# Optimization experiments

Measured on AMD Instinct MI355X. Metric: run time of the kernel, lower is better.

The kernel has to match this reference:

```python
import jax, jax.numpy as jnp
import numpy as np

B, S, D = 8, 4096, 64
NEG = 10000.0


def setup_inputs() -> dict:
    key = jax.random.key(0)
    k1, k2, k3, k4 = jax.random.split(key, 4)
    query = jax.random.normal(k1, (B, S, D), dtype=jnp.float32)
    k_ = jax.random.normal(k2, (B, S, D), dtype=jnp.float32)
    v_ = jax.random.normal(k3, (B, S, D), dtype=jnp.float32)
    # padding mask [B, Sk]: mostly valid, tail padded for some rows
    lens = jax.random.randint(k4, (B,), S // 2, S + 1)
    mask = jnp.arange(S)[None, :] < lens[:, None]
    return {"query": query, "key": k_, "value": v_, "mask": mask}


def reference(query, key, value, mask):
    d = query.shape[-1]
    scale = 1.0 / jnp.sqrt(jnp.asarray(d, dtype=query.dtype))
    # e: [B, Sq, Sk]
    e = jnp.einsum("bqd,bkd->bqk", query, key) * scale
    # causal (history_only) mask: key index > query index gets -10000
    q_idx = jnp.arange(query.shape[1])[:, None]
    k_idx = jnp.arange(key.shape[1])[None, :]
    e = e - NEG * (k_idx > q_idx).astype(e.dtype)[None, :, :]
    # padding mask [B, 1, Sk]
    e = e - NEG * (1.0 - mask.astype(e.dtype))[:, None, :]
    attention = jax.nn.softmax(e, axis=-1)
    return jnp.einsum("bqk,bkd->bqd", attention, value)
```

## Files before the change

kernel.cpp:

```cpp
#include <hip/hip_runtime.h>
#include <hip/hip_bf16.h>

#define B_N 8
#define S_N 4096
#define D_N 64
#define NQT 64
#define TILE_BYTES 8192
#define SLOT_BYTES 4352

typedef __attribute__((ext_vector_type(8))) short bf16x8;
typedef __attribute__((ext_vector_type(4))) float f32x4;
typedef __attribute__((ext_vector_type(16))) float f32x16;
typedef unsigned uint2v __attribute__((ext_vector_type(2)));
typedef unsigned uint4v __attribute__((ext_vector_type(4)));

__device__ __forceinline__ float fast_exp2(float x) {
#if __has_builtin(__builtin_amdgcn_exp2f)
  return __builtin_amdgcn_exp2f(x);
#else
  return exp2f(x);
#endif
}

__device__ __forceinline__ unsigned f2bf_u(float x) {
  __hip_bfloat16 h = __float2bfloat16(x);
  return (unsigned)__builtin_bit_cast(unsigned short, h);
}
__device__ __forceinline__ unsigned pack2(float a, float b) {
  return f2bf_u(a) | (f2bf_u(b) << 16);
}

__device__ __forceinline__ void pl32swap(unsigned& a, unsigned& b) {
#if __has_builtin(__builtin_amdgcn_permlane32_swap)
  uint2v r = __builtin_amdgcn_permlane32_swap(a, b, false, false);
  a = r[0];
  b = r[1];
#else
  asm volatile("v_permlane32_swap_b32 %0, %1" : "+v"(a), "+v"(b));
#endif
}
__device__ __forceinline__ float xhalf_sum(float x) {
  unsigned a = __builtin_bit_cast(unsigned, x), b = a;
  pl32swap(a, b);
  return __builtin_bit_cast(float, a) + __builtin_bit_cast(float, b);
}

__global__ void __launch_bounds__(256)
lens_kernel(const unsigned* __restrict__ mask, int* __restrict__ lens) {
  int b = blockIdx.x, tid = threadIdx.x;
  unsigned first = mask[0];
  int cnt = 0;
  if (first == 0x01010101u) {
    const unsigned char* m = ((const unsigned char*)mask) + (size_t)b * S_N;
    for (int i = tid; i < S_N; i += 256) cnt += (m[i] != 0);
  } else if (first == 0x3F800000u) {
    const float* m = ((const float*)mask) + (size_t)b * S_N;
    for (int i = tid; i < S_N; i += 256) cnt += (m[i] != 0.0f);
  } else {
    const int* m = ((const int*)mask) + (size_t)b * S_N;
    for (int i = tid; i < S_N; i += 256) cnt += (m[i] != 0);
  }
#pragma unroll
  for (int off = 32; off > 0; off >>= 1) cnt += __shfl_down(cnt, off);
  __shared__ int acc[4];
  if ((tid & 63) == 0) acc[tid >> 6] = cnt;
  __syncthreads();
  if (tid == 0) lens[b] = acc[0] + acc[1] + acc[2] + acc[3];
}

__global__ void __launch_bounds__(256)
prep_kernel(const float* __restrict__ K, const float* __restrict__ V,
            char* __restrict__ Ks, char* __restrict__ VTs) {
  __shared__ float vl[64][72];
  const int bt = blockIdx.x, tid = threadIdx.x;
  const float* Kt = K + (size_t)bt * 4096;
  const float* Vt = V + (size_t)bt * 4096;
  char* Ko = Ks + (size_t)bt * TILE_BYTES;
  char* Vo = VTs + (size_t)bt * TILE_BYTES;
#pragma unroll
  for (int i = 0; i < 2; ++i) {
    int c = tid + i * 256;
    int r = c >> 3, j = c & 7;
    f32x4 a = *(const f32x4*)(Kt + r * 64 + j * 8);
    f32x4 b4 = *(const f32x4*)(Kt + r * 64 + j * 8 + 4);
    union { bf16x8 v; unsigned u[4]; } pk;
    pk.u[0] = pack2(a[0], a[1]);   pk.u[1] = pack2(a[2], a[3]);
    pk.u[2] = pack2(b4[0], b4[1]); pk.u[3] = pack2(b4[2], b4[3]);
    *(bf16x8*)(Ko + ((r >> 5) * 4 + (j >> 1)) * 1024 + (j & 1) * 512 +
               (r & 31) * 16) = pk.v;
    f32x4 va = *(const f32x4*)(Vt + r * 64 + j * 8);
    f32x4 vb = *(const f32x4*)(Vt + r * 64 + j * 8 + 4);
#pragma unroll
    for (int e = 0; e < 4; ++e) vl[j * 8 + e][r] = va[e];
#pragma unroll
    for (int e = 0; e < 4; ++e) vl[j * 8 + 4 + e][r] = vb[e];
  }
  __syncthreads();
#pragma unroll
  for (int i = 0; i < 2; ++i) {
    int c = tid + i * 256;
    int d = c >> 3, j = c & 7;
    f32x4 fa = *(const f32x4*)(&vl[d][j * 8]);
    f32x4 fb = *(const f32x4*)(&vl[d][j * 8 + 4]);
    union { bf16x8 v; unsigned u[4]; } pk;
    pk.u[0] = pack2(fa[0], fa[1]); pk.u[1] = pack2(fa[2], fa[3]);
    pk.u[2] = pack2(fb[0], fb[1]); pk.u[3] = pack2(fb[2], fb[3]);
    *(bf16x8*)(Vo + ((d >> 5) * 4 + (j >> 1)) * 1024 + (j & 1) * 512 +
               (d & 31) * 16) = pk.v;
  }
}

__global__ void __launch_bounds__(256, 2)
attn_kernel(const float* __restrict__ Qg, const char* __restrict__ Ks,
            const char* __restrict__ VTs, const int* __restrict__ lens,
            float* __restrict__ Og, char* __restrict__ parts,
            int M, int U) {
  const int tid = threadIdx.x;
  const int lane = tid & 63;
  const int w = tid >> 6;
  const int bid = blockIdx.x;
  const int b = bid & 7;
  const int u2 = (bid >> 3) * 4 + w;
  const int ws = u2 & 1;
  const int u = (U - 1) - (u2 >> 1);
  int a = 0;
  while ((M * (a + 1) * (a + 2)) / 2 <= u) ++a;
  const int v = u - (M * a * (a + 1)) / 2;
  const int qt = a * M + v / (a + 1);
  const int s = v - (v / (a + 1)) * (a + 1);
  const int kq = a + 1;

  const int q0 = qt * 64;
  const int len = lens[b];
  int nt = (len + 63) >> 6;
  if (qt + 1 < nt) nt = qt + 1;
  const int beg = s * M;
  int cnt = nt - beg;
  if (cnt > M) cnt = M;
  if (cnt < 0) cnt = 0;

  const int q31 = lane & 31;
  const int h = lane >> 5;
  const int qg = q0 + ws * 32 + q31;

  const char* Kb = Ks + (size_t)(b * NQT) * TILE_BYTES;
  const char* Vb = VTs + (size_t)(b * NQT) * TILE_BYTES;

  constexpr float CS = 0.125f * 1.4426950408889634f;
  bf16x8 qf[4];
#pragma unroll
  for (int c = 0; c < 4; ++c) {
    const float* src = Qg + ((size_t)(b * S_N) + qg) * D_N + c * 16 + h * 8;
    f32x4 aa = *(const f32x4*)src;
    f32x4 b4 = *(const f32x4*)(src + 4);
    union { bf16x8 v; unsigned u[4]; } pk;
    pk.u[0] = pack2(aa[0] * CS, aa[1] * CS);
    pk.u[1] = pack2(aa[2] * CS, aa[3] * CS);
    pk.u[2] = pack2(b4[0] * CS, b4[1] * CS);
    pk.u[3] = pack2(b4[2] * CS, b4[3] * CS);
    qf[c] = pk.v;
  }

  f32x16 ot0 = {}, ot1 = {};
  float l = 0.0f;

  bf16x8 ka[8];
  if (cnt > 0) {
    const char* Kt = Kb + (size_t)beg * TILE_BYTES + lane * 16;
#pragma unroll
    for (int c = 0; c < 8; ++c) ka[c] = *(const bf16x8*)(Kt + c * 1024);
  }

  for (int j = 0; j < cnt; ++j) {
    const int t = beg + j;

    f32x16 s0, s1;
#pragma unroll
    for (int i = 0; i < 16; ++i) { s0[i] = -8.0f; s1[i] = -8.0f; }
#pragma unroll
    for (int c = 0; c < 4; ++c) {
      s0 = __builtin_amdgcn_mfma_f32_32x32x16_bf16(ka[c], qf[c], s0, 0, 0, 0);
      s1 = __builtin_amdgcn_mfma_f32_32x32x16_bf16(ka[4 + c], qf[c], s1, 0, 0, 0);
    }

    bf16x8 vv[8];
    const char* Vt2 = Vb + (size_t)t * TILE_BYTES + lane * 16;
#pragma unroll
    for (int c = 0; c < 8; ++c) vv[c] = *(const bf16x8*)(Vt2 + c * 1024);

    if (j + 1 < cnt) {
      const char* Kn = Kb + (size_t)(t + 1) * TILE_BYTES + lane * 16;
#pragma unroll
      for (int c = 0; c < 8; ++c) ka[c] = *(const bf16x8*)(Kn + c * 1024);
    }

    const int kv0 = t * 64;
    if (t == qt || kv0 + 64 > len) {
#pragma unroll
      for (int g = 0; g < 4; ++g)
#pragma unroll
        for (int jj = 0; jj < 4; ++jj) {
          int kl = 8 * g + 4 * h + jj;
          if (kv0 + kl > qg || kv0 + kl >= len) s0[g * 4 + jj] = -10000.0f;
          if (kv0 + 32 + kl > qg || kv0 + 32 + kl >= len) s1[g * 4 + jj] = -10000.0f;
        }
    }

    float ps0 = 0.f, ps1 = 0.f, ps2 = 0.f, ps3 = 0.f;
#pragma unroll
    for (int g = 0; g < 4; ++g) {
      s0[4 * g + 0] = fast_exp2(s0[4 * g + 0]); ps0 += s0[4 * g + 0];
      s0[4 * g + 1] = fast_exp2(s0[4 * g + 1]); ps1 += s0[4 * g + 1];
      s0[4 * g + 2] = fast_exp2(s0[4 * g + 2]); ps2 += s0[4 * g + 2];
      s0[4 * g + 3] = fast_exp2(s0[4 * g + 3]); ps3 += s0[4 * g + 3];
      s1[4 * g + 0] = fast_exp2(s1[4 * g + 0]); ps0 += s1[4 * g + 0];
      s1[4 * g + 1] = fast_exp2(s1[4 * g + 1]); ps1 += s1[4 * g + 1];
      s1[4 * g + 2] = fast_exp2(s1[4 * g + 2]); ps2 += s1[4 * g + 2];
      s1[4 * g + 3] = fast_exp2(s1[4 * g + 3]); ps3 += s1[4 * g + 3];
    }
    l += xhalf_sum((ps0 + ps1) + (ps2 + ps3));

    unsigned opk0[4][2], opk1[4][2];
#pragma unroll
    for (int g = 0; g < 4; ++g) {
      opk0[g][0] = pack2(s0[4 * g + 0], s0[4 * g + 1]);
      opk0[g][1] = pack2(s0[4 * g + 2], s0[4 * g + 3]);
      opk1[g][0] = pack2(s1[4 * g + 0], s1[4 * g + 1]);
      opk1[g][1] = pack2(s1[4 * g + 2], s1[4 * g + 3]);
    }
    bf16x8 pb[4];
#pragma unroll
    for (int c = 0; c < 4; ++c) {
      const unsigned(*o)[2] = (c < 2) ? opk0 : opk1;
      const int g0 = 2 * (c & 1), g1 = g0 + 1;
      unsigned a0 = o[g0][0], b0 = o[g1][0];
      unsigned a1 = o[g0][1], b1 = o[g1][1];
      pl32swap(a0, b0);
      pl32swap(a1, b1);
      union { bf16x8 v; unsigned u[4]; } pk;
      pk.u[0] = a0; pk.u[1] = a1; pk.u[2] = b0; pk.u[3] = b1;
      pb[c] = pk.v;
    }

#pragma unroll
    for (int c = 0; c < 4; ++c) {
      ot0 = __builtin_amdgcn_mfma_f32_32x32x16_bf16(vv[c], pb[c], ot0, 0, 0, 0);
      ot1 = __builtin_amdgcn_mfma_f32_32x32x16_bf16(vv[4 + c], pb[c], ot1, 0, 0, 0);
    }
  }

  if (kq == 1) {
    float linv = 1.0f / l;
    float* orow = Og + ((size_t)(b * S_N) + qg) * D_N;
#pragma unroll
    for (int g = 0; g < 4; ++g) {
      f32x4 oa = {ot0[4 * g + 0] * linv, ot0[4 * g + 1] * linv,
                  ot0[4 * g + 2] * linv, ot0[4 * g + 3] * linv};
      *(f32x4*)(orow + 8 * g + 4 * h) = oa;
      f32x4 ob = {ot1[4 * g + 0] * linv, ot1[4 * g + 1] * linv,
                  ot1[4 * g + 2] * linv, ot1[4 * g + 3] * linv};
      *(f32x4*)(orow + 32 + 8 * g + 4 * h) = ob;
    }
  } else {
    char* slot = parts + (((size_t)b * U + u) * 2 + ws) * SLOT_BYTES;
    unsigned wv[16];
#pragma unroll
    for (int jj = 0; jj < 8; ++jj) {
      wv[jj] = pack2(ot0[2 * jj], ot0[2 * jj + 1]);
      wv[8 + jj] = pack2(ot1[2 * jj], ot1[2 * jj + 1]);
    }
    uint4v* dst = (uint4v*)(slot + lane * 64);
#pragma unroll
    for (int q4 = 0; q4 < 4; ++q4)
      dst[q4] = (uint4v){wv[4 * q4], wv[4 * q4 + 1], wv[4 * q4 + 2], wv[4 * q4 + 3]};
    *(float*)(slot + 4096 + lane * 4) = l;
  }
}

__global__ void __launch_bounds__(128)
merge_kernel(const char* __restrict__ parts, float* __restrict__ Og,
             int M, int U) {
  const int bid = blockIdx.x;
  const int b = bid & 7, qt = bid >> 3;
  const int a = qt / M;
  const int kq = a + 1;
  if (kq == 1) return;
  const int tid = threadIdx.x;
  const int ws = tid >> 6;
  const int lane = tid & 63;
  const int base_u = (M * a * (a + 1)) / 2 + (qt - a * M) * (a + 1);

  float acc[32];
#pragma unroll
  for (int i = 0; i < 32; ++i) acc[i] = 0.0f;
  float L = 0.0f;
  for (int s2 = 0; s2 < kq; ++s2) {
    const char* slot =
        parts + (((size_t)b * U + base_u + s2) * 2 + ws) * SLOT_BYTES;
    const uint4v* src = (const uint4v*)(slot + lane * 64);
#pragma unroll
    for (int q4 = 0; q4 < 4; ++q4) {
      uint4v wv = src[q4];
#pragma unroll
      for (int e = 0; e < 4; ++e) {
        unsigned uw = wv[e];
        acc[2 * (4 * q4 + e)] += __builtin_bit_cast(float, uw << 16);
        acc[2 * (4 * q4 + e) + 1] += __builtin_bit_cast(float, uw & 0xFFFF0000u);
      }
    }
    L += *(const float*)(slot + 4096 + lane * 4);
  }
  float linv = 1.0f / L;
  const int q31 = lane & 31;
  const int h = lane >> 5;
  float* orow = Og + ((size_t)(b * S_N) + qt * 64 + ws * 32 + q31) * D_N;
#pragma unroll
  for (int dt = 0; dt < 2; ++dt)
#pragma unroll
    for (int g = 0; g < 4; ++g) {
      f32x4 w = {acc[dt * 16 + 4 * g + 0] * linv, acc[dt * 16 + 4 * g + 1] * linv,
                 acc[dt * 16 + 4 * g + 2] * linv, acc[dt * 16 + 4 * g + 3] * linv};
      *(f32x4*)(orow + dt * 32 + 8 * g + 4 * h) = w;
    }
}

extern "C" void kernel_launch(void* const* d_in, const int* in_sizes, int n_in,
                              void* d_out, int out_size, void* d_ws, size_t ws_size,
                              hipStream_t stream) {
  const float* Qg = (const float*)d_in[0];
  const float* Kg = (const float*)d_in[1];
  const float* Vg = (const float*)d_in[2];
  const unsigned* mask = (const unsigned*)d_in[3];
  float* Og = (float*)d_out;

  int* lens = (int*)d_ws;
  char* Ks = (char*)d_ws + 4096;
  char* VTs = Ks + (size_t)B_N * NQT * TILE_BYTES;
  char* parts = VTs + (size_t)B_N * NQT * TILE_BYTES;

  int M = 8, U = 288;
  size_t need = 4096 + ((size_t)2 * B_N * NQT * TILE_BYTES) +
                (size_t)B_N * 288 * 2 * SLOT_BYTES;
  if (ws_size < need) { M = 64; U = 64; }

  lens_kernel<<<dim3(B_N), dim3(256), 0, stream>>>(mask, lens);
  prep_kernel<<<dim3(B_N * NQT), dim3(256), 0, stream>>>(Kg, Vg, Ks, VTs);
  attn_kernel<<<dim3(B_N * U / 2), dim3(256), 0, stream>>>(Qg, Ks, VTs, lens,
                                                           Og, parts, M, U);
  if (M == 8)
    merge_kernel<<<dim3(B_N * NQT), dim3(128), 0, stream>>>(parts, Og, M, U);
}
```

Before: 54.72 us.

## Double-buffer K and V tiles in registers and raise priority around MFMAs

The loop now prefetches both the next K and the next V tile into alternate register sets (ping-pong buffers) one iteration ahead, instead of loading V synchronously inside the iteration. The aim is to hide global-load latency of V behind the softmax and MFMA work. It also wraps the MFMA blocks in s_setprio to favour matrix issue across waves. The extra 16 bf16x8 registers raise VGPR pressure and may reduce occupancy or cause spills.

```diff
diff --git a/kernel.cpp b/kernel.cpp
--- a/kernel.cpp
+++ b/kernel.cpp
@@ -164,34 +164,40 @@
   f32x16 ot0 = {}, ot1 = {};
   float l = 0.0f;
 
-  bf16x8 ka[8];
+  bf16x8 kA[8], vA[8], kB[8], vB[8];
   if (cnt > 0) {
     const char* Kt = Kb + (size_t)beg * TILE_BYTES + lane * 16;
-#pragma unroll
-    for (int c = 0; c < 8; ++c) ka[c] = *(const bf16x8*)(Kt + c * 1024);
-  }
-
-  for (int j = 0; j < cnt; ++j) {
+    const char* Vt = Vb + (size_t)beg * TILE_BYTES + lane * 16;
+#pragma unroll
+    for (int c = 0; c < 8; ++c) {
+      kA[c] = *(const bf16x8*)(Kt + c * 1024);
+      vA[c] = *(const bf16x8*)(Vt + c * 1024);
+    }
+  }
+
+  auto body = [&](bf16x8(&kc)[8], bf16x8(&vc)[8], bf16x8(&kn)[8],
+                  bf16x8(&vn)[8], int j) __attribute__((always_inline)) {
     const int t = beg + j;
 
     f32x16 s0, s1;
 #pragma unroll
     for (int i = 0; i < 16; ++i) { s0[i] = -8.0f; s1[i] = -8.0f; }
+    __builtin_amdgcn_s_setprio(1);
 #pragma unroll
     for (int c = 0; c < 4; ++c) {
-      s0 = __builtin_amdgcn_mfma_f32_32x32x16_bf16(ka[c], qf[c], s0, 0, 0, 0);
-      s1 = __builtin_amdgcn_mfma_f32_32x32x16_bf16(ka[4 + c], qf[c], s1, 0, 0, 0);
-    }
-
-    bf16x8 vv[8];
-    const char* Vt2 = Vb + (size_t)t * TILE_BYTES + lane * 16;
-#pragma unroll
-    for (int c = 0; c < 8; ++c) vv[c] = *(const bf16x8*)(Vt2 + c * 1024);
+      s0 = __builtin_amdgcn_mfma_f32_32x32x16_bf16(kc[c], qf[c], s0, 0, 0, 0);
+      s1 = __builtin_amdgcn_mfma_f32_32x32x16_bf16(kc[4 + c], qf[c], s1, 0, 0, 0);
+    }
+    __builtin_amdgcn_s_setprio(0);
 
     if (j + 1 < cnt) {
       const char* Kn = Kb + (size_t)(t + 1) * TILE_BYTES + lane * 16;
-#pragma unroll
-      for (int c = 0; c < 8; ++c) ka[c] = *(const bf16x8*)(Kn + c * 1024);
+      const char* Vn = Vb + (size_t)(t + 1) * TILE_BYTES + lane * 16;
+#pragma unroll
+      for (int c = 0; c < 8; ++c) {
+        kn[c] = *(const bf16x8*)(Kn + c * 1024);
+        vn[c] = *(const bf16x8*)(Vn + c * 1024);
+      }
     }
 
     const int kv0 = t * 64;
@@ -242,11 +248,20 @@
       pb[c] = pk.v;
     }
 
+    __builtin_amdgcn_s_setprio(1);
 #pragma unroll
     for (int c = 0; c < 4; ++c) {
-      ot0 = __builtin_amdgcn_mfma_f32_32x32x16_bf16(vv[c], pb[c], ot0, 0, 0, 0);
-      ot1 = __builtin_amdgcn_mfma_f32_32x32x16_bf16(vv[4 + c], pb[c], ot1, 0, 0, 0);
-    }
+      ot0 = __builtin_amdgcn_mfma_f32_32x32x16_bf16(vc[c], pb[c], ot0, 0, 0, 0);
+      ot1 = __builtin_amdgcn_mfma_f32_32x32x16_bf16(vc[4 + c], pb[c], ot1, 0, 0, 0);
+    }
+    __builtin_amdgcn_s_setprio(0);
+  };
+
+  for (int j = 0; j < cnt; ++j) {
+    if ((j & 1) == 0)
+      body(kA, vA, kB, vB, j);
+    else
+      body(kB, vB, kA, vA, j);
   }
 
   if (kq == 1) {
```

Result: slower. 119.4 us (+118.1%).
